# Performance work log

Measured on AMD Instinct MI355X. Metric: run time of the kernel, lower is better.

Reference implementation:

```python
import jax, jax.numpy as jnp
import numpy as np

B, F, H, C, K = 4096, 1536, 256, 38, 7  # nodes, feat_dim(effnet_b3), hidden, classes, knn k
EPS = 1e-5  # BatchNorm eps


def setup_inputs() -> dict:
    key = jax.random.key(0)
    ks = jax.random.split(key, 20)
    r = lambda i, shape, s=1.0: jax.random.normal(ks[i], shape, jnp.float32) * s
    u = lambda i, shape: jax.random.uniform(ks[i], shape, jnp.float32, 0.5, 1.5)
    inp = {
        "features": r(0, (B, F)),          # CNN backbone output
        "noise": r(1, (B, B)),             # tie-break noise (scaled by 1e-6 inside)
        # BatchNorm1d on CNN features (eval mode: running stats)
        "bnf_g": jnp.ones((F,)), "bnf_b": jnp.zeros((F,)),
        "bnf_m": r(2, (F,), 0.1), "bnf_v": u(3, (F,)),
        # GCNConv weights
        "W1": r(4, (F, H), 0.02), "b1": jnp.zeros((H,)),
        "W2": r(5, (H, H), 0.05), "b2": jnp.zeros((H,)),
        "W3": r(6, (H, H), 0.05), "b3": jnp.zeros((H,)),
        # PyG BatchNorms (eval mode)
        "bn1_g": jnp.ones((H,)), "bn1_b": jnp.zeros((H,)), "bn1_m": r(7, (H,), 0.1), "bn1_v": u(8, (H,)),
        "bn2_g": jnp.ones((H,)), "bn2_b": jnp.zeros((H,)), "bn2_m": r(9, (H,), 0.1), "bn2_v": u(10, (H,)),
        "bn3_g": jnp.ones((H,)), "bn3_b": jnp.zeros((H,)), "bn3_m": r(11, (H,), 0.1), "bn3_v": u(12, (H,)),
        # classifier MLP
        "Wc1": r(13, (H + F, H // 2), 0.02), "bc1": jnp.zeros((H // 2,)),
        "Wc2": r(14, (H // 2, C), 0.05), "bc2": jnp.zeros((C,)),
    }
    return inp


def _bn(x, g, b, m, v):
    return (x - m) * jax.lax.rsqrt(v + EPS) * g + b


def _knn_edges(x, noise):
    # torch.cdist (p=2) + 1e-6 noise + topk smallest; drop self (col 0)
    sq = jnp.sum(x * x, axis=1)
    d2 = jnp.maximum(sq[:, None] + sq[None, :] - 2.0 * (x @ x.T), 0.0)
    d = jnp.sqrt(d2) + noise * 1e-6
    _, idx = jax.lax.top_k(-d, K + 1)          # smallest K+1 distances
    knn = idx[:, 1:]                           # [B, K] neighbors (col 0 = self)
    src = jnp.repeat(jnp.arange(B), K)         # edge i -> j as in edge_list [[i, j]]
    dst = knn.reshape(-1)
    return src, dst


def _gcn(x, src, dst, W, b):
    # GCNConv: add self-loops, symmetric normalization, aggregate at target (dst)
    h = x @ W
    loop = jnp.arange(B)
    s = jnp.concatenate([src, loop])
    t = jnp.concatenate([dst, loop])
    deg = jnp.zeros((B,), x.dtype).at[t].add(1.0)
    dinv = jax.lax.rsqrt(deg)                  # deg >= 1 due to self-loops
    norm = dinv[s] * dinv[t]
    out = jnp.zeros_like(h).at[t].add(norm[:, None] * h[s])
    return out + b


def reference(features, noise, bnf_g, bnf_b, bnf_m, bnf_v,
              W1, b1, W2, b2, W3, b3,
              bn1_g, bn1_b, bn1_m, bn1_v,
              bn2_g, bn2_b, bn2_m, bn2_v,
              bn3_g, bn3_b, bn3_m, bn3_v,
              Wc1, bc1, Wc2, bc2):
    # CNN head: BN (eval) + dropout(identity in eval)
    x = _bn(features, bnf_g, bnf_b, bnf_m, bnf_v)
    src, dst = _knn_edges(jax.lax.stop_gradient(x), noise)
    x_orig = x
    h = jax.nn.relu(_bn(_gcn(x, src, dst, W1, b1), bn1_g, bn1_b, bn1_m, bn1_v))
    h = jax.nn.relu(_bn(_gcn(h, src, dst, W2, b2), bn2_g, bn2_b, bn2_m, bn2_v))
    h = _bn(_gcn(h, src, dst, W3, b3), bn3_g, bn3_b, bn3_m, bn3_v)
    # batch = arange(B) => global_mean_pool is identity per node
    comb = jnp.concatenate([h, x_orig], axis=1)        # [B, H+F]
    hid = jax.nn.relu(comb @ Wc1 + bc1)
    return hid @ Wc2 + bc2                             # [B, num_classes]
```

## Files before the change

### kernel.cpp

```cpp
#include <hip/hip_runtime.h>
#include <hip/hip_bf16.h>
#include <math.h>

#define Bn 4096
#define Fn 1536
#define Hn 256
#define Cn 38
#define Kn 7
#define GBK 64

typedef __attribute__((ext_vector_type(8))) short short8;
typedef __attribute__((ext_vector_type(4))) float f32x4;
typedef unsigned long long u64;
typedef unsigned int u32;
typedef unsigned short u16;

__device__ __forceinline__ void gld16(const void* g, void* l) {
  __builtin_amdgcn_global_load_lds((const __attribute__((address_space(1))) unsigned int*)g,
                                   (__attribute__((address_space(3))) unsigned int*)l, 16, 0, 0);
}

__global__ void k_prep(const float* __restrict__ g, const float* __restrict__ b,
                       const float* __restrict__ m, const float* __restrict__ v,
                       double* __restrict__ A64, double* __restrict__ C64) {
  int f = blockIdx.x * 256 + threadIdx.x;
  if (f < Fn) {
    double rs = 1.0 / sqrt((double)v[f] + 1e-5);
    double a = (double)g[f] * rs;
    A64[f] = a;
    C64[f] = (double)b[f] - (double)m[f] * a;
  }
}

__global__ void k_bnsplit(const float* __restrict__ feat, const double* __restrict__ A64,
                          const double* __restrict__ C64,
                          u16* __restrict__ Ah, u16* __restrict__ Al, double* __restrict__ sq) {
  int row = blockIdx.x;
  int f0 = threadIdx.x * 8;
  const float* fr = feat + (size_t)row * Fn + f0;
  float4 a = *reinterpret_cast<const float4*>(fr);
  float4 b = *reinterpret_cast<const float4*>(fr + 4);
  float xs[8] = {a.x, a.y, a.z, a.w, b.x, b.y, b.z, b.w};
  short8 hv, lv;
  double ss = 0.0;
#pragma unroll
  for (int k = 0; k < 8; k++) {
    double xd = fma((double)xs[k], A64[f0 + k], C64[f0 + k]);
    ss = fma(xd, xd, ss);
    float x = (float)xd;
    __hip_bfloat16 h = __float2bfloat16(x);
    float hf = __bfloat162float(h);
    __hip_bfloat16 lo = __float2bfloat16(x - hf);
    hv[k] = (short)*reinterpret_cast<u16*>(&h);
    lv[k] = (short)*reinterpret_cast<u16*>(&lo);
  }
  *reinterpret_cast<short8*>(Ah + (size_t)row * Fn + f0) = hv;
  *reinterpret_cast<short8*>(Al + (size_t)row * Fn + f0) = lv;
#pragma unroll
  for (int o = 32; o; o >>= 1) ss += __shfl_down(ss, o);
  __shared__ double red[3];
  if ((threadIdx.x & 63) == 0) red[threadIdx.x >> 6] = ss;
  __syncthreads();
  if (threadIdx.x == 0) sq[row] = red[0] + red[1] + red[2];
}

__global__ void k_wsplit(const float* __restrict__ W, int K, int N,
                         u16* __restrict__ Wth, u16* __restrict__ Wtl) {
  __shared__ float t[32][33];
  int k0 = blockIdx.y * 32, n0 = blockIdx.x * 32;
  int tx = threadIdx.x & 31, ty = threadIdx.x >> 5;
  for (int p = 0; p < 32; p += 8) {
    int k = k0 + ty + p, n = n0 + tx;
    t[ty + p][tx] = (k < K && n < N) ? W[(size_t)k * N + n] : 0.f;
  }
  __syncthreads();
  for (int p = 0; p < 32; p += 8) {
    int n = n0 + ty + p, k = k0 + tx;
    if (n < N && k < K) {
      float x = t[tx][ty + p];
      __hip_bfloat16 h = __float2bfloat16(x);
      float hf = __bfloat162float(h);
      __hip_bfloat16 lo = __float2bfloat16(x - hf);
      Wth[(size_t)n * K + k] = *reinterpret_cast<u16*>(&h);
      Wtl[(size_t)n * K + k] = *reinterpret_cast<u16*>(&lo);
    }
  }
}

__global__ __launch_bounds__(256) void k_gram(
    const u16* __restrict__ Ah, const double* __restrict__ sq, u64* __restrict__ part) {
  __shared__ union {
    u16 t[2][2][8192];
    float c2[128 * 65];
  } lds;
  const int tid = threadIdx.x;
  const int w = tid >> 6, l = tid & 63;
  int swz = (blockIdx.x & 7) * 66 + (blockIdx.x >> 3);
  int rem = swz, ti = 0;
#pragma unroll 1
  while (rem >= 32 - ti) { rem -= 32 - ti; ti++; }
  const int tj = ti + rem;
  const int rA0 = ti * 128, rB0 = tj * 128;
  const int isDiag = (ti == tj);

  f32x4 acc[4][4];
  const f32x4 fz = {0.f, 0.f, 0.f, 0.f};
#pragma unroll
  for (int i = 0; i < 4; i++)
#pragma unroll
    for (int j = 0; j < 4; j++) acc[i][j] = fz;

  const u16* mats[2] = { Ah + (size_t)rA0 * Fn, Ah + (size_t)rB0 * Fn };

  auto stage = [&](int buf, int k0) {
#pragma unroll
    for (int q = 0; q < 8; q++) {
      int idx = w * 8 + q;
      int mm = idx >> 4, kh = (idx >> 3) & 1, s = idx & 7;
      int row = s * 16 + (l >> 2);
      int colel = ((l & 3) * 8) ^ ((row & 8) ? 16 : 0);
      gld16(mats[mm] + (size_t)row * Fn + k0 + kh * 32 + colel,
            (char*)&lds.t[buf][mm][0] + kh * 8192 + s * 1024);
    }
  };

  const int swzr = (l & 8) ? 32 : 0;
  const int cB = ((l >> 4) * 16) ^ swzr;

  stage(0, 0);
  const int NT = Fn / GBK;
  int cur = 0;
  for (int kt = 0; kt < NT; kt++) {
    __syncthreads();
    if (kt + 1 < NT) stage(cur ^ 1, (kt + 1) * GBK);
#pragma unroll
    for (int kh = 0; kh < 2; kh++) {
      short8 fa[4], fb[4];
#pragma unroll
      for (int i = 0; i < 4; i++) {
        int ar = (w >> 1) * 64 + i * 16 + (l & 15);
        fa[i] = *reinterpret_cast<const short8*>((const char*)&lds.t[cur][0][0] + kh * 8192 + ar * 64 + cB);
        int br = (w & 1) * 64 + i * 16 + (l & 15);
        fb[i] = *reinterpret_cast<const short8*>((const char*)&lds.t[cur][1][0] + kh * 8192 + br * 64 + cB);
      }
#pragma unroll
      for (int i = 0; i < 4; i++)
#pragma unroll
        for (int j = 0; j < 4; j++)
          acc[i][j] = __builtin_amdgcn_mfma_f32_16x16x32_bf16(fa[i], fb[j], acc[i][j], 0, 0, 0);
    }
    cur ^= 1;
  }
  __syncthreads();

  const int fr = l & 15, fq = l >> 4;
#pragma unroll 1
  for (int p = 0; p < 2; p++) {
    if ((w & 1) == p) {
#pragma unroll
      for (int i = 0; i < 4; i++) {
        int r0 = (w >> 1) * 64 + i * 16 + fq * 4;
#pragma unroll
        for (int j = 0; j < 4; j++) {
          int c0 = j * 16 + fr;
#pragma unroll
          for (int gg = 0; gg < 4; gg++)
            lds.c2[(r0 + gg) * 65 + c0] = acc[i][j][gg];
        }
      }
    }
    __syncthreads();
    u64 top[8];
#pragma unroll
    for (int k = 0; k < 8; k++) top[k] = ~0ull;
    int prow = -1, slot = 0;
    if (tid < 128) {
      int grow = rA0 + tid;
      float sqr = (float)sq[grow];
#pragma unroll 1
      for (int c = 0; c < 64; c++) {
        int gc = rB0 + p * 64 + c;
        if (gc == grow) continue;
        float gv = lds.c2[tid * 65 + c];
        float d2 = fmaxf(sqr + (float)sq[gc] - 2.f * gv, 0.f);
        u64 key = ((u64)__float_as_uint(d2) << 32) | (u32)gc;
        if (key < top[7]) {
          top[7] = key;
#pragma unroll
          for (int k = 7; k > 0; k--)
            if (top[k] < top[k - 1]) { u64 tmp = top[k]; top[k] = top[k - 1]; top[k - 1] = tmp; }
        }
      }
      prow = grow; slot = tj * 2 + p;
    } else if (!isDiag) {
      int idx = tid - 128, cl = idx >> 1, q = idx & 1;
      int gcol = rB0 + p * 64 + cl;
      float sqc = (float)sq[gcol];
#pragma unroll 1
      for (int s = 0; s < 64; s++) {
        int rr = q * 64 + s;
        float gv = lds.c2[rr * 65 + cl];
        int gr = rA0 + rr;
        float d2 = fmaxf(sqc + (float)sq[gr] - 2.f * gv, 0.f);
        u64 key = ((u64)__float_as_uint(d2) << 32) | (u32)gr;
        if (key < top[7]) {
          top[7] = key;
#pragma unroll
          for (int k = 7; k > 0; k--)
            if (top[k] < top[k - 1]) { u64 tmp = top[k]; top[k] = top[k - 1]; top[k - 1] = tmp; }
        }
      }
      prow = gcol; slot = ti * 2 + q;
    }
    if (prow >= 0) {
      u64* dst = part + ((size_t)prow * 64 + slot) * 8;
#pragma unroll
      for (int k = 0; k < 8; k++) dst[k] = top[k];
    }
    __syncthreads();
  }
}

__global__ __launch_bounds__(256) void k_candmerge(const u64* __restrict__ part,
                                                   int* __restrict__ cand) {
  int row = blockIdx.x * 4 + (threadIdx.x >> 6);
  int l = threadIdx.x & 63;
  const u64* p = part + (size_t)row * 512 + (size_t)l * 8;
  u64 e[8];
#pragma unroll
  for (int k = 0; k < 8; k++) e[k] = p[k];
#pragma unroll 1
  for (int rnd = 0; rnd < 16; rnd++) {
    u64 m = e[0];
#pragma unroll
    for (int k = 1; k < 8; k++) m = e[k] < m ? e[k] : m;
#pragma unroll
    for (int off = 32; off; off >>= 1) {
      u64 o = __shfl_xor(m, off);
      m = o < m ? o : m;
    }
    if (l == 0) cand[row * 16 + rnd] = (int)(u32)m;
#pragma unroll
    for (int k = 0; k < 8; k++)
      if (e[k] == m) e[k] = ~0ull;
  }
}

__global__ __launch_bounds__(256) void k_rerank(
    const float* __restrict__ feat, const double* __restrict__ A64,
    const double* __restrict__ C64, const double* __restrict__ sq,
    const float* __restrict__ noise, const int* __restrict__ cand,
    int* __restrict__ knn, float* __restrict__ deg) {
  int row = blockIdx.x;
  int w = threadIdx.x >> 6, l = threadIdx.x & 63;
  double xr[Fn / 64];
  const float* fr = feat + (size_t)row * Fn;
#pragma unroll
  for (int i = 0; i < Fn / 64; i++) {
    int e = l + 64 * i;
    xr[i] = fma((double)fr[e], A64[e], C64[e]);
  }
  __shared__ double dots[16];
  for (int m = w; m < 16; m += 4) {
    int c = cand[row * 16 + m];
    const float* fc = feat + (size_t)c * Fn;
    double s = 0.0;
#pragma unroll
    for (int i = 0; i < Fn / 64; i++) {
      int e = l + 64 * i;
      double xj = fma((double)fc[e], A64[e], C64[e]);
      s = fma(xr[i], xj, s);
    }
#pragma unroll
    for (int off = 32; off; off >>= 1) s += __shfl_xor(s, off);
    if (l == 0) dots[m] = s;
  }
  __syncthreads();
  if (threadIdx.x == 0) {
    double sr = sq[row];
    double bd[Kn]; int bi7[Kn];
#pragma unroll
    for (int k = 0; k < Kn; k++) { bd[k] = 1e300; bi7[k] = 0; }
#pragma unroll 1
    for (int m = 0; m < 16; m++) {
      int c = cand[row * 16 + m];
      double d2 = sr + sq[c] - 2.0 * dots[m];
      d2 = d2 > 0.0 ? d2 : 0.0;
      double d = sqrt(d2) + (double)noise[(size_t)row * Bn + c] * 1e-6;
      if (d < bd[Kn - 1]) {
        bd[Kn - 1] = d; bi7[Kn - 1] = c;
#pragma unroll
        for (int k = Kn - 1; k > 0; k--)
          if (bd[k] < bd[k - 1]) {
            double td = bd[k]; bd[k] = bd[k - 1]; bd[k - 1] = td;
            int ti = bi7[k]; bi7[k] = bi7[k - 1]; bi7[k - 1] = ti;
          }
      }
    }
#pragma unroll
    for (int k = 0; k < Kn; k++) {
      knn[row * Kn + k] = bi7[k];
      atomicAdd(&deg[bi7[k]], 1.f);
    }
  }
}

__global__ void k_deginit(float* __restrict__ deg) {
  int i = blockIdx.x * 256 + threadIdx.x;
  if (i < Bn) deg[i] = 1.f;
}
__global__ void k_dinv(const float* __restrict__ deg, float* __restrict__ dinv) {
  int i = blockIdx.x * 256 + threadIdx.x;
  if (i < Bn) dinv[i] = rsqrtf(deg[i]);
}

__global__ void k_aggsc(const float* __restrict__ h, const int* __restrict__ knn,
                        const float* __restrict__ dinv, float* __restrict__ out) {
  int s = blockIdx.x, f = threadIdx.x;
  float hv = h[(size_t)s * Hn + f] * dinv[s];
#pragma unroll
  for (int k = 0; k < Kn; k++) {
    int t = knn[s * Kn + k];
    atomicAdd(&out[(size_t)t * Hn + f], dinv[t] * hv);
  }
}

__global__ void k_bnact_split(const float* __restrict__ x, const float* __restrict__ g,
                              const float* __restrict__ b, const float* __restrict__ m,
                              const float* __restrict__ v, int relu,
                              u16* __restrict__ oh, u16* __restrict__ ol) {
  size_t i8 = ((size_t)blockIdx.x * 256 + threadIdx.x) * 8;
  int c0 = (int)(i8 & (Hn - 1));
  float4 a = *reinterpret_cast<const float4*>(x + i8);
  float4 bb = *reinterpret_cast<const float4*>(x + i8 + 4);
  float xs[8] = {a.x, a.y, a.z, a.w, bb.x, bb.y, bb.z, bb.w};
  short8 hv, lv;
#pragma unroll
  for (int k = 0; k < 8; k++) {
    int c = c0 + k;
    float val = (xs[k] - m[c]) * rsqrtf(v[c] + 1e-5f) * g[c] + b[c];
    if (relu) val = fmaxf(val, 0.f);
    __hip_bfloat16 h = __float2bfloat16(val);
    float hf = __bfloat162float(h);
    __hip_bfloat16 lo = __float2bfloat16(val - hf);
    hv[k] = (short)*reinterpret_cast<u16*>(&h);
    lv[k] = (short)*reinterpret_cast<u16*>(&lo);
  }
  *reinterpret_cast<short8*>(oh + i8) = hv;
  *reinterpret_cast<short8*>(ol + i8) = lv;
}

__global__ __launch_bounds__(256) void k_mgemm(
    const u16* __restrict__ Ah1, const u16* __restrict__ Al1, int lda1,
    const u16* __restrict__ Ah2, const u16* __restrict__ Al2, int lda2, int Ksplit,
    const u16* __restrict__ Wth, const u16* __restrict__ Wtl,
    const float* __restrict__ bias, float* __restrict__ C, int N, int K, int ep,
    float* __restrict__ C2, const float* __restrict__ dinvp,
    u16* __restrict__ OH, u16* __restrict__ OL) {
  __shared__ u16 tA[2][2][4096];
  __shared__ u16 tB[2][2][4096];
  const int tid = threadIdx.x;
  const int w = tid >> 6, l = tid & 63;
  const int m0 = blockIdx.y * 64, n0 = blockIdx.x * 64;
  const int fr = l & 15, fq = l >> 4;

  f32x4 acc[2][2];
  const f32x4 fz = {0.f, 0.f, 0.f, 0.f};
#pragma unroll
  for (int i = 0; i < 2; i++)
#pragma unroll
    for (int j = 0; j < 2; j++) acc[i][j] = fz;

  auto stage = [&](int buf, int k0) {
#pragma unroll
    for (int q = 0; q < 2; q++) {
      int s = w * 2 + q;
      int kg = k0 + s * 8;
      const u16* ah; const u16* al; int ld; int kk = kg;
      if (kg < Ksplit) { ah = Ah1; al = Al1; ld = lda1; }
      else             { ah = Ah2; al = Al2; ld = lda2; kk = kg - Ksplit; }
      gld16(ah + (size_t)(m0 + l) * ld + kk, (char*)&tA[buf][0][0] + s * 1024);
      gld16(al + (size_t)(m0 + l) * ld + kk, (char*)&tA[buf][1][0] + s * 1024);
      gld16(Wth + (size_t)(n0 + l) * K + kg, (char*)&tB[buf][0][0] + s * 1024);
      gld16(Wtl + (size_t)(n0 + l) * K + kg, (char*)&tB[buf][1][0] + s * 1024);
    }
  };

  stage(0, 0);
  const int NT = K / GBK;
  int cur = 0;
  for (int kt = 0; kt < NT; kt++) {
    __syncthreads();
    if (kt + 1 < NT) stage(cur ^ 1, (kt + 1) * GBK);
#pragma unroll
    for (int kh = 0; kh < 2; kh++) {
      const int kb = (kh * 4 + fq) * 1024;
      short8 fa[2][2], fb[2][2];
#pragma unroll
      for (int i = 0; i < 2; i++) {
        int ar = (w >> 1) * 32 + i * 16 + fr;
        fa[0][i] = *reinterpret_cast<const short8*>((const char*)&tA[cur][0][0] + kb + ar * 16);
        fa[1][i] = *reinterpret_cast<const short8*>((const char*)&tA[cur][1][0] + kb + ar * 16);
        int br = (w & 1) * 32 + i * 16 + fr;
        fb[0][i] = *reinterpret_cast<const short8*>((const char*)&tB[cur][0][0] + kb + br * 16);
        fb[1][i] = *reinterpret_cast<const short8*>((const char*)&tB[cur][1][0] + kb + br * 16);
      }
#pragma unroll
      for (int i = 0; i < 2; i++)
#pragma unroll
        for (int j = 0; j < 2; j++) {
          acc[i][j] = __builtin_amdgcn_mfma_f32_16x16x32_bf16(fa[1][i], fb[0][j], acc[i][j], 0, 0, 0);
          acc[i][j] = __builtin_amdgcn_mfma_f32_16x16x32_bf16(fa[0][i], fb[1][j], acc[i][j], 0, 0, 0);
          acc[i][j] = __builtin_amdgcn_mfma_f32_16x16x32_bf16(fa[0][i], fb[0][j], acc[i][j], 0, 0, 0);
        }
    }
    cur ^= 1;
  }

#pragma unroll
  for (int i = 0; i < 2; i++) {
    int rg0 = m0 + (w >> 1) * 32 + i * 16 + fq * 4;
#pragma unroll
    for (int j = 0; j < 2; j++) {
      int cg = n0 + (w & 1) * 32 + j * 16 + fr;
      if (cg >= N) continue;
      float bv = (ep >= 1) ? bias[cg] : 0.f;
#pragma unroll
      for (int g = 0; g < 4; g++) {
        float raw = acc[i][j][g];
        size_t idx = (size_t)(rg0 + g) * N + cg;
        if (ep == 3) {
          float di = dinvp[rg0 + g];
          C[idx] = raw;
          C2[idx] = di * di * raw + bv;
        } else if (ep == 4) {
          float val = fmaxf(raw + bv, 0.f);
          __hip_bfloat16 h = __float2bfloat16(val);
          float hf = __bfloat162float(h);
          __hip_bfloat16 lo = __float2bfloat16(val - hf);
          OH[idx] = *reinterpret_cast<u16*>(&h);
          OL[idx] = *reinterpret_cast<u16*>(&lo);
        } else {
          float val = raw + bv;
          if (ep == 2) val = fmaxf(val, 0.f);
          C[idx] = val;
        }
      }
    }
  }
}

extern "C" void kernel_launch(void* const* d_in, const int* in_sizes, int n_in,
                              void* d_out, int out_size, void* d_ws, size_t ws_size,
                              hipStream_t stream) {
  const float* feat  = (const float*)d_in[0];
  const float* noise = (const float*)d_in[1];
  const float* bnf_g = (const float*)d_in[2];
  const float* bnf_b = (const float*)d_in[3];
  const float* bnf_m = (const float*)d_in[4];
  const float* bnf_v = (const float*)d_in[5];
  const float* W1 = (const float*)d_in[6];
  const float* b1 = (const float*)d_in[7];
  const float* W2 = (const float*)d_in[8];
  const float* b2 = (const float*)d_in[9];
  const float* W3 = (const float*)d_in[10];
  const float* b3 = (const float*)d_in[11];
  const float* bn1_g = (const float*)d_in[12];
  const float* bn1_b = (const float*)d_in[13];
  const float* bn1_m = (const float*)d_in[14];
  const float* bn1_v = (const float*)d_in[15];
  const float* bn2_g = (const float*)d_in[16];
  const float* bn2_b = (const float*)d_in[17];
  const float* bn2_m = (const float*)d_in[18];
  const float* bn2_v = (const float*)d_in[19];
  const float* bn3_g = (const float*)d_in[20];
  const float* bn3_b = (const float*)d_in[21];
  const float* bn3_m = (const float*)d_in[22];
  const float* bn3_v = (const float*)d_in[23];
  const float* Wc1 = (const float*)d_in[24];
  const float* bc1 = (const float*)d_in[25];
  const float* Wc2 = (const float*)d_in[26];
  const float* bc2 = (const float*)d_in[27];
  float* outp = (float*)d_out;

  char* w = (char*)d_ws;
  size_t off = 0;
  auto alloc = [&](size_t n) { void* p = w + off; off = (off + n + 255) & ~(size_t)255; return p; };
  u16*    Ahb  = (u16*)   alloc((size_t)Bn * Fn * 2);
  u16*    Alb  = (u16*)   alloc((size_t)Bn * Fn * 2);
  double* A64  = (double*)alloc(Fn * 8);
  double* C64  = (double*)alloc(Fn * 8);
  double* sq   = (double*)alloc(Bn * 8);
  u64*    part = (u64*)   alloc((size_t)Bn * 64 * 8 * 8);
  int*    cand = (int*)   alloc((size_t)Bn * 16 * 4);
  int*    knn  = (int*)   alloc((size_t)Bn * Kn * 4);
  float*  deg  = (float*) alloc(Bn * 4);
  float*  dinv = (float*) alloc(Bn * 4);
  float*  g1   = (float*) alloc((size_t)Bn * Hn * 4);
  float*  g2   = (float*) alloc((size_t)Bn * Hn * 4);
  u16*    sh   = (u16*)   alloc((size_t)Bn * Hn * 2);
  u16*    sl   = (u16*)   alloc((size_t)Bn * Hn * 2);
  u16*    hidh = (u16*)   alloc((size_t)Bn * 128 * 2);
  u16*    hidl = (u16*)   alloc((size_t)Bn * 128 * 2);
  u16*    W1th = (u16*)   alloc((size_t)Fn * Hn * 2);
  u16*    W1tl = (u16*)   alloc((size_t)Fn * Hn * 2);
  u16*    W2th = (u16*)   alloc((size_t)Hn * Hn * 2);
  u16*    W2tl = (u16*)   alloc((size_t)Hn * Hn * 2);
  u16*    W3th = (u16*)   alloc((size_t)Hn * Hn * 2);
  u16*    W3tl = (u16*)   alloc((size_t)Hn * Hn * 2);
  u16*    Wc1th= (u16*)   alloc((size_t)(Hn + Fn) * 128 * 2);
  u16*    Wc1tl= (u16*)   alloc((size_t)(Hn + Fn) * 128 * 2);
  u16*    Wc2th= (u16*)   alloc((size_t)64 * 128 * 2);
  u16*    Wc2tl= (u16*)   alloc((size_t)64 * 128 * 2);
  (void)ws_size; (void)in_sizes; (void)n_in; (void)out_size;

  k_prep<<<(Fn + 255) / 256, 256, 0, stream>>>(bnf_g, bnf_b, bnf_m, bnf_v, A64, C64);
  k_bnsplit<<<Bn, Fn / 8, 0, stream>>>(feat, A64, C64, Ahb, Alb, sq);
  k_wsplit<<<dim3(Hn / 32, Fn / 32), 256, 0, stream>>>(W1, Fn, Hn, W1th, W1tl);
  k_wsplit<<<dim3(Hn / 32, Hn / 32), 256, 0, stream>>>(W2, Hn, Hn, W2th, W2tl);
  k_wsplit<<<dim3(Hn / 32, Hn / 32), 256, 0, stream>>>(W3, Hn, Hn, W3th, W3tl);
  k_wsplit<<<dim3(128 / 32, (Hn + Fn) / 32), 256, 0, stream>>>(Wc1, Hn + Fn, 128, Wc1th, Wc1tl);
  k_wsplit<<<dim3(2, 4), 256, 0, stream>>>(Wc2, 128, Cn, Wc2th, Wc2tl);

  k_gram<<<528, 256, 0, stream>>>(Ahb, sq, part);
  k_candmerge<<<Bn / 4, 256, 0, stream>>>(part, cand);
  k_deginit<<<(Bn + 255) / 256, 256, 0, stream>>>(deg);
  k_rerank<<<Bn, 256, 0, stream>>>(feat, A64, C64, sq, noise, cand, knn, deg);
  k_dinv<<<(Bn + 255) / 256, 256, 0, stream>>>(deg, dinv);

  dim3 gm(Hn / 64, Bn / 64);
  k_mgemm<<<gm, 256, 0, stream>>>(Ahb, Alb, Fn, Ahb, Alb, Fn, Fn, W1th, W1tl, b1, g1, Hn, Fn, 3,
                                  g2, dinv, nullptr, nullptr);
  k_aggsc<<<Bn, Hn, 0, stream>>>(g1, knn, dinv, g2);
  k_bnact_split<<<(Bn * Hn) / (256 * 8), 256, 0, stream>>>(g2, bn1_g, bn1_b, bn1_m, bn1_v, 1, sh, sl);
  k_mgemm<<<gm, 256, 0, stream>>>(sh, sl, Hn, sh, sl, Hn, Hn, W2th, W2tl, b2, g1, Hn, Hn, 3,
                                  g2, dinv, nullptr, nullptr);
  k_aggsc<<<Bn, Hn, 0, stream>>>(g1, knn, dinv, g2);
  k_bnact_split<<<(Bn * Hn) / (256 * 8), 256, 0, stream>>>(g2, bn2_g, bn2_b, bn2_m, bn2_v, 1, sh, sl);
  k_mgemm<<<gm, 256, 0, stream>>>(sh, sl, Hn, sh, sl, Hn, Hn, W3th, W3tl, b3, g1, Hn, Hn, 3,
                                  g2, dinv, nullptr, nullptr);
  k_aggsc<<<Bn, Hn, 0, stream>>>(g1, knn, dinv, g2);
  k_bnact_split<<<(Bn * Hn) / (256 * 8), 256, 0, stream>>>(g2, bn3_g, bn3_b, bn3_m, bn3_v, 0, sh, sl);
  k_mgemm<<<dim3(128 / 64, Bn / 64), 256, 0, stream>>>(sh, sl, Hn, Ahb, Alb, Fn, Hn,
                                                       Wc1th, Wc1tl, bc1, nullptr, 128, Hn + Fn, 4,
                                                       nullptr, nullptr, hidh, hidl);
  k_mgemm<<<dim3(1, Bn / 64), 256, 0, stream>>>(hidh, hidl, 128, hidh, hidl, 128, 128,
                                                Wc2th, Wc2tl, bc2, outp, Cn, 128, 1,
                                                nullptr, nullptr, nullptr, nullptr);
}
```

Measured before the change: 614.9 us.

## Shrink Gram kernel tiles to 64x64 and drop LDS double buffering

The symmetric Gram/top-k kernel now uses 64x64 tiles instead of 128x128, raising the block count from 528 to 2080 upper-triangle tiles. The LDS double buffer is removed and staging is done synchronously after compute, shrinking LDS use so more blocks fit per CU. The epilogue becomes a single pass where 64 threads do row top-k and 64 do column top-k, writing one partial slot per 64-column tile. In exchange, global operand traffic roughly doubles, the copy no longer overlaps compute, and only half the threads do top-k work.

```diff
diff --git a/kernel.cpp b/kernel.cpp
--- a/kernel.cpp
+++ b/kernel.cpp
@@ -90,134 +90,124 @@
 __global__ __launch_bounds__(256) void k_gram(
     const u16* __restrict__ Ah, const double* __restrict__ sq, u64* __restrict__ part) {
   __shared__ union {
-    u16 t[2][2][8192];
-    float c2[128 * 65];
+    u16 t[2][4096];
+    float c[64 * 65];
   } lds;
   const int tid = threadIdx.x;
   const int w = tid >> 6, l = tid & 63;
-  int swz = (blockIdx.x & 7) * 66 + (blockIdx.x >> 3);
+  int swz = (blockIdx.x & 7) * 260 + (blockIdx.x >> 3);
   int rem = swz, ti = 0;
 #pragma unroll 1
-  while (rem >= 32 - ti) { rem -= 32 - ti; ti++; }
+  while (rem >= 64 - ti) { rem -= 64 - ti; ti++; }
   const int tj = ti + rem;
-  const int rA0 = ti * 128, rB0 = tj * 128;
+  const int rA0 = ti * 64, rB0 = tj * 64;
   const int isDiag = (ti == tj);
 
-  f32x4 acc[4][4];
+  f32x4 acc[2][2];
   const f32x4 fz = {0.f, 0.f, 0.f, 0.f};
 #pragma unroll
-  for (int i = 0; i < 4; i++)
-#pragma unroll
-    for (int j = 0; j < 4; j++) acc[i][j] = fz;
+  for (int i = 0; i < 2; i++)
+#pragma unroll
+    for (int j = 0; j < 2; j++) acc[i][j] = fz;
 
   const u16* mats[2] = { Ah + (size_t)rA0 * Fn, Ah + (size_t)rB0 * Fn };
 
-  auto stage = [&](int buf, int k0) {
-#pragma unroll
-    for (int q = 0; q < 8; q++) {
-      int idx = w * 8 + q;
-      int mm = idx >> 4, kh = (idx >> 3) & 1, s = idx & 7;
+  auto stage = [&](int k0) {
+#pragma unroll
+    for (int q = 0; q < 4; q++) {
+      int idx = w * 4 + q;
+      int mm = idx >> 3, kh = (idx >> 2) & 1, s = idx & 3;
       int row = s * 16 + (l >> 2);
       int colel = ((l & 3) * 8) ^ ((row & 8) ? 16 : 0);
       gld16(mats[mm] + (size_t)row * Fn + k0 + kh * 32 + colel,
-            (char*)&lds.t[buf][mm][0] + kh * 8192 + s * 1024);
+            (char*)&lds.t[mm][0] + kh * 4096 + s * 1024);
     }
   };
 
-  const int swzr = (l & 8) ? 32 : 0;
-  const int cB = ((l >> 4) * 16) ^ swzr;
-
-  stage(0, 0);
+  const int cB = ((l >> 4) * 16) ^ ((l & 8) ? 32 : 0);
+  const int fr16 = l & 15;
+
+  stage(0);
   const int NT = Fn / GBK;
-  int cur = 0;
   for (int kt = 0; kt < NT; kt++) {
     __syncthreads();
-    if (kt + 1 < NT) stage(cur ^ 1, (kt + 1) * GBK);
 #pragma unroll
     for (int kh = 0; kh < 2; kh++) {
-      short8 fa[4], fb[4];
-#pragma unroll
-      for (int i = 0; i < 4; i++) {
-        int ar = (w >> 1) * 64 + i * 16 + (l & 15);
-        fa[i] = *reinterpret_cast<const short8*>((const char*)&lds.t[cur][0][0] + kh * 8192 + ar * 64 + cB);
-        int br = (w & 1) * 64 + i * 16 + (l & 15);
-        fb[i] = *reinterpret_cast<const short8*>((const char*)&lds.t[cur][1][0] + kh * 8192 + br * 64 + cB);
+      short8 fa[2], fb[2];
+#pragma unroll
+      for (int i = 0; i < 2; i++) {
+        int ar = (w >> 1) * 32 + i * 16 + fr16;
+        fa[i] = *reinterpret_cast<const short8*>((const char*)&lds.t[0][0] + kh * 4096 + ar * 64 + cB);
+        int br = (w & 1) * 32 + i * 16 + fr16;
+        fb[i] = *reinterpret_cast<const short8*>((const char*)&lds.t[1][0] + kh * 4096 + br * 64 + cB);
       }
 #pragma unroll
-      for (int i = 0; i < 4; i++)
-#pragma unroll
-        for (int j = 0; j < 4; j++)
+      for (int i = 0; i < 2; i++)
+#pragma unroll
+        for (int j = 0; j < 2; j++)
           acc[i][j] = __builtin_amdgcn_mfma_f32_16x16x32_bf16(fa[i], fb[j], acc[i][j], 0, 0, 0);
     }
-    cur ^= 1;
+    __syncthreads();
+    if (kt + 1 < NT) stage((kt + 1) * GBK);
+  }
+
+  const int fr = l & 15, fq = l >> 4;
+#pragma unroll
+  for (int i = 0; i < 2; i++) {
+    int r0 = (w >> 1) * 32 + i * 16 + fq * 4;
+#pragma unroll
+    for (int j = 0; j < 2; j++) {
+      int c0 = (w & 1) * 32 + j * 16 + fr;
+#pragma unroll
+      for (int gg = 0; gg < 4; gg++)
+        lds.c[(r0 + gg) * 65 + c0] = acc[i][j][gg];
+    }
   }
   __syncthreads();
 
-  const int fr = l & 15, fq = l >> 4;
+  u64 top[8];
+#pragma unroll
+  for (int k = 0; k < 8; k++) top[k] = ~0ull;
+  if (tid < 64) {
+    int grow = rA0 + tid;
+    float sqr = (float)sq[grow];
 #pragma unroll 1
-  for (int p = 0; p < 2; p++) {
-    if ((w & 1) == p) {
-#pragma unroll
-      for (int i = 0; i < 4; i++) {
-        int r0 = (w >> 1) * 64 + i * 16 + fq * 4;
-#pragma unroll
-        for (int j = 0; j < 4; j++) {
-          int c0 = j * 16 + fr;
-#pragma unroll
-          for (int gg = 0; gg < 4; gg++)
-            lds.c2[(r0 + gg) * 65 + c0] = acc[i][j][gg];
-        }
+    for (int c = 0; c < 64; c++) {
+      int gc = rB0 + c;
+      if (gc == grow) continue;
+      float gv = lds.c[tid * 65 + c];
+      float d2 = fmaxf(sqr + (float)sq[gc] - 2.f * gv, 0.f);
+      u64 key = ((u64)__float_as_uint(d2) << 32) | (u32)gc;
+      if (key < top[7]) {
+        top[7] = key;
+#pragma unroll
+        for (int k = 7; k > 0; k--)
+          if (top[k] < top[k - 1]) { u64 tmp = top[k]; top[k] = top[k - 1]; top[k - 1] = tmp; }
       }
     }
-    __syncthreads();
-    u64 top[8];
-#pragma unroll
-    for (int k = 0; k < 8; k++) top[k] = ~0ull;
-    int prow = -1, slot = 0;
-    if (tid < 128) {
-      int grow = rA0 + tid;
-      float sqr = (float)sq[grow];
+    u64* dst = part + ((size_t)grow * 64 + tj) * 8;
+#pragma unroll
+    for (int k = 0; k < 8; k++) dst[k] = top[k];
+  } else if (tid < 128 && !isDiag) {
+    int cl = tid - 64;
+    int gcol = rB0 + cl;
+    float sqc = (float)sq[gcol];
 #pragma unroll 1
-      for (int c = 0; c < 64; c++) {
-        int gc = rB0 + p * 64 + c;
-        if (gc == grow) continue;
-        float gv = lds.c2[tid * 65 + c];
-        float d2 = fmaxf(sqr + (float)sq[gc] - 2.f * gv, 0.f);
-        u64 key = ((u64)__float_as_uint(d2) << 32) | (u32)gc;
-        if (key < top[7]) {
-          top[7] = key;
-#pragma unroll
-          for (int k = 7; k > 0; k--)
-            if (top[k] < top[k - 1]) { u64 tmp = top[k]; top[k] = top[k - 1]; top[k - 1] = tmp; }
-        }
+    for (int s = 0; s < 64; s++) {
+      float gv = lds.c[s * 65 + cl];
+      int gr = rA0 + s;
+      float d2 = fmaxf(sqc + (float)sq[gr] - 2.f * gv, 0.f);
+      u64 key = ((u64)__float_as_uint(d2) << 32) | (u32)gr;
+      if (key < top[7]) {
+        top[7] = key;
+#pragma unroll
+        for (int k = 7; k > 0; k--)
+          if (top[k] < top[k - 1]) { u64 tmp = top[k]; top[k] = top[k - 1]; top[k - 1] = tmp; }
       }
-      prow = grow; slot = tj * 2 + p;
-    } else if (!isDiag) {
-      int idx = tid - 128, cl = idx >> 1, q = idx & 1;
-      int gcol = rB0 + p * 64 + cl;
-      float sqc = (float)sq[gcol];
-#pragma unroll 1
-      for (int s = 0; s < 64; s++) {
-        int rr = q * 64 + s;
-        float gv = lds.c2[rr * 65 + cl];
-        int gr = rA0 + rr;
-        float d2 = fmaxf(sqc + (float)sq[gr] - 2.f * gv, 0.f);
-        u64 key = ((u64)__float_as_uint(d2) << 32) | (u32)gr;
-        if (key < top[7]) {
-          top[7] = key;
-#pragma unroll
-          for (int k = 7; k > 0; k--)
-            if (top[k] < top[k - 1]) { u64 tmp = top[k]; top[k] = top[k - 1]; top[k - 1] = tmp; }
-        }
-      }
-      prow = gcol; slot = ti * 2 + q;
-    }
-    if (prow >= 0) {
-      u64* dst = part + ((size_t)prow * 64 + slot) * 8;
-#pragma unroll
-      for (int k = 0; k < 8; k++) dst[k] = top[k];
-    }
-    __syncthreads();
+    }
+    u64* dst = part + ((size_t)gcol * 64 + ti) * 8;
+#pragma unroll
+    for (int k = 0; k < 8; k++) dst[k] = top[k];
   }
 }
 
@@ -522,7 +512,7 @@
   k_wsplit<<<dim3(128 / 32, (Hn + Fn) / 32), 256, 0, stream>>>(Wc1, Hn + Fn, 128, Wc1th, Wc1tl);
   k_wsplit<<<dim3(2, 4), 256, 0, stream>>>(Wc2, 128, Cn, Wc2th, Wc2tl);
 
-  k_gram<<<528, 256, 0, stream>>>(Ahb, sq, part);
+  k_gram<<<2080, 256, 0, stream>>>(Ahb, sq, part);
   k_candmerge<<<Bn / 4, 256, 0, stream>>>(part, cand);
   k_deginit<<<(Bn + 255) / 256, 256, 0, stream>>>(deg);
   k_rerank<<<Bn, 256, 0, stream>>>(feat, A64, C64, sq, noise, cand, knn, deg);
```

Result: faster. 554.7 us (-9.8%).
